# Kernel tuning notes

Hardware: AMD Instinct MI355X
Metric: run time of the kernel (lower is better)

Reference implementation:

```python
import jax, jax.numpy as jnp
import numpy as np

H, W, WS = 48, 48, 8          # spatial grid and window radius
D, NUM_HEADS = 256, 8          # embed dim, heads
N = H * W
K = (2 * WS + 1) ** 2          # max neighbors = 289
EPS = 1e-5


def _precompute_neighbors(h, w, ws):
    """Faithful port of SCAM._precompute_neighbors (pads ragged rows with n[0])."""
    neighbors_list = []
    for idx in range(h * w):
        row, col = idx // w, idx % w
        nb = []
        for i in range(-ws, ws + 1):
            for j in range(-ws, ws + 1):
                r, c = row + i, col + j
                if 0 <= r < h and 0 <= c < w:
                    nb.append(r * w + c)
        neighbors_list.append(nb)
    max_n = max(len(n) for n in neighbors_list)
    padded = np.array([n + [n[0]] * (max_n - len(n)) for n in neighbors_list], dtype=np.int32)
    return padded


def setup_inputs() -> dict:
    key = jax.random.key(0)
    k1, k2, k3, k4 = jax.random.split(key, 4)
    B = 1
    scale = 0.02
    return {
        "x1": jax.random.normal(k1, (B, N, D), dtype=jnp.float32),
        "x2": jax.random.normal(k2, (B, N, D), dtype=jnp.float32),
        "ln_gamma": jnp.ones((D,), jnp.float32),
        "ln_beta": jnp.zeros((D,), jnp.float32),
        "in_proj_w": jax.random.normal(k3, (3 * D, D), dtype=jnp.float32) * scale,
        "in_proj_b": jnp.zeros((3 * D,), jnp.float32),
        "out_w": jax.random.normal(k4, (D, D), dtype=jnp.float32) * scale,
        "out_b": jnp.zeros((D,), jnp.float32),
        "neighbors_idx": jnp.asarray(_precompute_neighbors(H, W, WS)),  # [N, K] int32
    }


def _layernorm(x, gamma, beta):
    mu = jnp.mean(x, axis=-1, keepdims=True)
    var = jnp.var(x, axis=-1, keepdims=True)
    return (x - mu) * jax.lax.rsqrt(var + EPS) * gamma + beta


def reference(x1, x2, ln_gamma, ln_beta, in_proj_w, in_proj_b, out_w, out_b, neighbors_idx):
    B, n, d = x1.shape
    hd = d // NUM_HEADS

    # --- neighborhood gather-attention on x2 ---
    neighbor_feats = x2[:, neighbors_idx, :]                         # [B, N, K, D]
    scores = jnp.einsum('bnd,bnkd->bnk', x2, neighbor_feats) / (d ** 0.5)
    attn_w = jax.nn.softmax(scores, axis=-1)                          # softmax over neighbors
    x2_fused = jnp.einsum('bnk,bnkd->bnd', attn_w, neighbor_feats)    # [B, N, D]
    x2_fused = _layernorm(x2_fused, ln_gamma, ln_beta)

    # --- standard MHA: query=x2_fused, key=value=x1 ---
    wq, wk, wv = in_proj_w[:d], in_proj_w[d:2 * d], in_proj_w[2 * d:]
    bq, bk, bv = in_proj_b[:d], in_proj_b[d:2 * d], in_proj_b[2 * d:]
    q = (x2_fused @ wq.T + bq).reshape(B, n, NUM_HEADS, hd).transpose(0, 2, 1, 3)
    k = (x1 @ wk.T + bk).reshape(B, n, NUM_HEADS, hd).transpose(0, 2, 1, 3)
    v = (x1 @ wv.T + bv).reshape(B, n, NUM_HEADS, hd).transpose(0, 2, 1, 3)
    logits = jnp.einsum('bhqd,bhkd->bhqk', q, k) / (hd ** 0.5)        # [B, H, N, N]
    p = jax.nn.softmax(logits, axis=-1)
    o = jnp.einsum('bhqk,bhkd->bhqd', p, v)                           # [B, H, N, hd]
    o = o.transpose(0, 2, 1, 3).reshape(B, n, d)
    return o @ out_w.T + out_b
```

## Files before the change

### kernel.cpp

```cpp
#include <hip/hip_runtime.h>
#include <math.h>

#define N 2304
#define D 256
#define K_NB 289
#define NH 8
#define HD 32
#define KS 8
#define SEG (N / KS)
#define NGR 2320

typedef __attribute__((ext_vector_type(8))) short short8;
typedef __attribute__((ext_vector_type(4))) short bf16x4;
typedef __attribute__((ext_vector_type(4))) float floatx4;

static __device__ __forceinline__ unsigned short f2bf(float x) {
  union { float f; unsigned u; } v; v.f = x;
  unsigned r = (v.u + 0x7fffu + ((v.u >> 16) & 1u)) >> 16;
  return (unsigned short)r;
}
static __device__ __forceinline__ unsigned pack2bf(float lo, float hi) {
  return (unsigned)f2bf(lo) | ((unsigned)f2bf(hi) << 16);
}

__global__ __launch_bounds__(256) void prep_kernel(
    const float* __restrict__ x2, unsigned short* __restrict__ x2b_full,
    unsigned short* __restrict__ x2t_full)
{
  __shared__ unsigned short T[16][17];
  const int tx = threadIdx.x & 15;
  const int ty = threadIdx.x >> 4;
  const int k0 = blockIdx.x * 16;
  const int f0 = blockIdx.y * 16;
  const int key = k0 + ty - 8;
  unsigned short v = 0;
  if (key >= 0 && key < N) v = f2bf(x2[(size_t)key * D + f0 + tx]);
  x2b_full[(size_t)(k0 + ty) * D + f0 + tx] = v;
  T[ty][tx] = v;
  __syncthreads();
  x2t_full[(size_t)(f0 + ty) * NGR + k0 + tx] = T[tx][ty];
}

__global__ __launch_bounds__(256) void stage1_mfma_kernel(
    const unsigned short* __restrict__ x2b,
    const unsigned short* __restrict__ x2t,
    const float* __restrict__ gamma, const float* __restrict__ beta,
    float* __restrict__ x2f)
{
  __shared__ float S[16][548];
  __shared__ __align__(16) unsigned short Pb[16][552];
  __shared__ float dinv[16];
  __shared__ float lr1[4][16], lr2[4][16];

  const int t    = threadIdx.x;
  const int w    = t >> 6;
  const int lane = t & 63;
  const int g    = lane >> 4;
  const int cL   = lane & 15;
  const int b  = blockIdx.x;
  const int r  = b / 3;
  const int c0 = (b % 3) * 16;
  const int qbase = r * 48 + c0;
  const int row_lo = max(0, 8 - r);
  const int row_hi = min(16, 55 - r);

  short8 qf[8];
  {
    const unsigned short* qptr = x2b + (size_t)(qbase + cL) * D + g * 8;
    #pragma unroll
    for (int s = 0; s < 8; ++s) qf[s] = *(const short8*)(qptr + s * 32);
  }

  for (int wr = row_lo + w; wr <= row_hi; wr += 4) {
    const int kr = r - 8 + wr;
    const int keybase = kr * 48 + c0 - 8;
    #pragma unroll
    for (int ch = 0; ch < 2; ++ch) {
      const unsigned short* kptr = x2b + (size_t)(keybase + ch * 16 + cL) * D + g * 8;
      floatx4 sa = {0.f, 0.f, 0.f, 0.f};
      #pragma unroll
      for (int s = 0; s < 8; ++s) {
        const short8 kf = *(const short8*)(kptr + s * 32);
        sa = __builtin_amdgcn_mfma_f32_16x16x32_bf16(qf[s], kf, sa, 0, 0, 0);
      }
      #pragma unroll
      for (int reg = 0; reg < 4; ++reg)
        S[g * 4 + reg][wr * 32 + ch * 16 + cL] = sa[reg] * 0.0625f;
    }
  }
  __syncthreads();

  if (t < 16) {
    const int c = c0 + t;
    const int nrows = min(r + 8, 47) - max(r - 8, 0) + 1;
    const int ncols = min(c + 8, 47) - max(c - 8, 0) + 1;
    const int mult  = K_NB - nrows * ncols + 1;
    if (mult > 1) {
      const int wr0 = max(0, 8 - r);
      const int wc0 = (c >= 8) ? t : (8 - c0);
      S[t][wr0 * 32 + wc0] += __logf((float)mult);
    }
  }
  __syncthreads();

  {
    const int qi = t >> 4, ti = t & 15;
    float ssum = 0.f;
    for (int wk = ti; wk < 544; wk += 16) {
      const int wr = wk >> 5, wc = wk & 31;
      const int kr = r - 8 + wr;
      const int kc = c0 - 8 + wc;
      const bool valid = (kr >= 0) & (kr < 48) & (kc >= 0) & (kc < 48) &
                         (wc >= qi) & (wc <= qi + 16);
      const float p = valid ? __expf(S[qi][wk]) : 0.f;
      ssum += p;
      Pb[qi][wk] = valid ? f2bf(p) : (unsigned short)0;
    }
    #pragma unroll
    for (int off = 1; off <= 8; off <<= 1) ssum += __shfl_xor(ssum, off);
    if (ti == 0) dinv[qi] = 1.f / ssum;
  }
  __syncthreads();

  floatx4 acc[4];
  #pragma unroll
  for (int ng = 0; ng < 4; ++ng) acc[ng] = (floatx4){0.f, 0.f, 0.f, 0.f};
  const int fb = w * 64;
  for (int wr = row_lo; wr <= row_hi; ++wr) {
    const int keybase = (r - 8 + wr) * 48 + c0 - 8;
    const short8 pA = *(const short8*)&Pb[cL][wr * 32 + g * 8];
    #pragma unroll
    for (int ng = 0; ng < 4; ++ng) {
      const short8 vf = *(const short8*)(x2t + (size_t)(fb + ng * 16 + cL) * NGR + keybase + g * 8);
      acc[ng] = __builtin_amdgcn_mfma_f32_16x16x32_bf16(pA, vf, acc[ng], 0, 0, 0);
    }
  }

  float vout[4][4], ps1[4] = {0,0,0,0}, ps2[4] = {0,0,0,0};
  #pragma unroll
  for (int reg = 0; reg < 4; ++reg) {
    const float di = dinv[g * 4 + reg];
    #pragma unroll
    for (int ng = 0; ng < 4; ++ng) {
      const float v = acc[ng][reg] * di;
      vout[ng][reg] = v;
      ps1[reg] += v;
      ps2[reg] += v * v;
    }
  }
  #pragma unroll
  for (int off = 1; off <= 8; off <<= 1) {
    #pragma unroll
    for (int reg = 0; reg < 4; ++reg) {
      ps1[reg] += __shfl_xor(ps1[reg], off);
      ps2[reg] += __shfl_xor(ps2[reg], off);
    }
  }
  if (cL == 0) {
    #pragma unroll
    for (int reg = 0; reg < 4; ++reg) {
      lr1[w][g * 4 + reg] = ps1[reg];
      lr2[w][g * 4 + reg] = ps2[reg];
    }
  }
  __syncthreads();
  #pragma unroll
  for (int reg = 0; reg < 4; ++reg) {
    const int m = g * 4 + reg;
    const float s1 = lr1[0][m] + lr1[1][m] + lr1[2][m] + lr1[3][m];
    const float s2 = lr2[0][m] + lr2[1][m] + lr2[2][m] + lr2[3][m];
    const float mu  = s1 * (1.f / 256.f);
    const float var = s2 * (1.f / 256.f) - mu * mu;
    const float rs  = rsqrtf(var + 1e-5f);
    #pragma unroll
    for (int ng = 0; ng < 4; ++ng) {
      const int f = fb + ng * 16 + cL;
      x2f[(size_t)(qbase + m) * D + f] = (vout[ng][reg] - mu) * rs * gamma[f] + beta[f];
    }
  }
}

__global__ __launch_bounds__(256) void gemm_qkv_kernel(
    const float* __restrict__ A0, const float* __restrict__ A1,
    const float* __restrict__ W, const float* __restrict__ bias,
    unsigned short* __restrict__ Qb, unsigned short* __restrict__ Kb,
    unsigned short* __restrict__ Vtb)
{
  __shared__ float As[64][68];
  __shared__ float Ws[64][68];
  const int t  = threadIdx.x;
  const int tx = t & 15;
  const int ty = t >> 4;
  const int j0 = blockIdx.x * 64;
  const int m0 = blockIdx.y * 64;
  const float* __restrict__ Asrc = (j0 < 256) ? A0 : A1;

  float acc[4][4];
  #pragma unroll
  for (int r = 0; r < 4; ++r)
    #pragma unroll
    for (int c = 0; c < 4; ++c) acc[r][c] = 0.f;

  for (int kc = 0; kc < D; kc += 64) {
    const int col = tx * 4;
    #pragma unroll
    for (int i = 0; i < 4; ++i) {
      const int r = ty + 16 * i;
      *(float4*)&As[r][col] = *(const float4*)(Asrc + (size_t)(m0 + r) * D + kc + col);
      *(float4*)&Ws[r][col] = *(const float4*)(W    + (size_t)(j0 + r) * D + kc + col);
    }
    __syncthreads();
    #pragma unroll 4
    for (int kk = 0; kk < 64; kk += 4) {
      float4 a4[4], b4[4];
      #pragma unroll
      for (int r = 0; r < 4; ++r) a4[r] = *(const float4*)&As[ty * 4 + r][kk];
      #pragma unroll
      for (int c = 0; c < 4; ++c) b4[c] = *(const float4*)&Ws[tx + 16 * c][kk];
      #pragma unroll
      for (int r = 0; r < 4; ++r)
        #pragma unroll
        for (int c = 0; c < 4; ++c) {
          acc[r][c] += a4[r].x * b4[c].x;
          acc[r][c] += a4[r].y * b4[c].y;
          acc[r][c] += a4[r].z * b4[c].z;
          acc[r][c] += a4[r].w * b4[c].w;
        }
    }
    __syncthreads();
  }
  const float qscale = 0.17677669529663687f;
  #pragma unroll
  for (int r = 0; r < 4; ++r) {
    const int m = m0 + ty * 4 + r;
    #pragma unroll
    for (int c = 0; c < 4; ++c) {
      const int j = j0 + tx + 16 * c;
      const float v = acc[r][c] + bias[j];
      if (j0 < 256)       Qb[(size_t)m * D + j] = f2bf(v * qscale);
      else if (j0 < 512)  Kb[(size_t)m * D + (j - 256)] = f2bf(v);
      else                Vtb[(size_t)(j - 512) * N + m] = f2bf(v);
    }
  }
}

__global__ __launch_bounds__(128) void attn_mfma_kernel(
    const unsigned short* __restrict__ Qb, const unsigned short* __restrict__ Kb,
    const unsigned short* __restrict__ Vtb,
    float* __restrict__ pacc, float* __restrict__ psum)
{
  __shared__ __align__(16) unsigned short Ksh[2][32 * 40];
  __shared__ __align__(16) unsigned short Vsh[2][32 * 40];

  const int t    = threadIdx.x;
  const int wv   = t >> 6;
  const int lane = t & 63;
  const int g    = lane >> 4;
  const int c    = lane & 15;
  const int seg  = blockIdx.x;
  const int qb   = blockIdx.y;
  const int head = blockIdx.z;
  const int q0w  = qb * 128 + wv * 64;
  const int key0 = seg * SEG;

  short8 qf[4];
  #pragma unroll
  for (int qt = 0; qt < 4; ++qt)
    qf[qt] = *(const short8*)(Qb + (size_t)(q0w + qt * 16 + c) * D + head * HD + g * 8);

  const unsigned short* ksrc = Kb  + (size_t)(key0 + t / 4) * D + head * HD + (t % 4) * 8;
  const unsigned short* vsrc = Vtb + (size_t)(head * HD + t / 4) * N + key0 + (t % 4) * 8;
  const int sdst = (t / 4) * 40 + (t % 4) * 8;

  {
    const float4 gk = *(const float4*)ksrc;
    const float4 gv = *(const float4*)vsrc;
    *(float4*)&Ksh[0][sdst] = gk;
    *(float4*)&Vsh[0][sdst] = gv;
  }
  __syncthreads();

  floatx4 accL[4], accH[4];
  float ssum[4];
  #pragma unroll
  for (int qt = 0; qt < 4; ++qt) {
    accL[qt] = (floatx4){0.f, 0.f, 0.f, 0.f};
    accH[qt] = (floatx4){0.f, 0.f, 0.f, 0.f};
    ssum[qt] = 0.f;
  }

  const int NCH = SEG / 32;
  for (int ch = 0; ch < NCH; ++ch) {
    float4 gk, gv;
    const bool more = (ch + 1 < NCH);
    if (more) {
      gk = *(const float4*)(ksrc + (size_t)(ch + 1) * 32 * D);
      gv = *(const float4*)(vsrc + (ch + 1) * 32);
    }
    const unsigned short* kb = Ksh[ch & 1];
    const unsigned short* vb = Vsh[ch & 1];

    #pragma unroll
    for (int kk = 0; kk < 2; ++kk) {
      const short8 kf  = *(const short8*)&kb[(kk * 16 + c) * 40 + g * 8];
      const bf16x4 vf0 = *(const bf16x4*)&vb[c * 40 + kk * 16 + g * 4];
      const bf16x4 vf1 = *(const bf16x4*)&vb[(16 + c) * 40 + kk * 16 + g * 4];
      #pragma unroll
      for (int qt = 0; qt < 4; ++qt) {
        const floatx4 z = {0.f, 0.f, 0.f, 0.f};
        floatx4 sA = __builtin_amdgcn_mfma_f32_16x16x32_bf16(kf, qf[qt], z, 0, 0, 0);
        const float p0 = __expf(sA[0]);
        const float p1 = __expf(sA[1]);
        const float p2 = __expf(sA[2]);
        const float p3 = __expf(sA[3]);
        ssum[qt] += (p0 + p1) + (p2 + p3);
        union { unsigned u[2]; bf16x4 s; } pB;
        pB.u[0] = pack2bf(p0, p1);
        pB.u[1] = pack2bf(p2, p3);
        accL[qt] = __builtin_amdgcn_mfma_f32_16x16x16bf16_1k(vf0, pB.s, accL[qt], 0, 0, 0);
        accH[qt] = __builtin_amdgcn_mfma_f32_16x16x16bf16_1k(vf1, pB.s, accH[qt], 0, 0, 0);
      }
    }
    if (more) {
      *(float4*)&Ksh[(ch + 1) & 1][sdst] = gk;
      *(float4*)&Vsh[(ch + 1) & 1][sdst] = gv;
    }
    __syncthreads();
  }

  #pragma unroll
  for (int qt = 0; qt < 4; ++qt) {
    float s = ssum[qt];
    s += __shfl_xor(s, 16);
    s += __shfl_xor(s, 32);
    const size_t row = (size_t)(seg * NH + head) * N + q0w + qt * 16 + c;
    *(float4*)(pacc + row * HD + g * 4) =
        make_float4(accL[qt][0], accL[qt][1], accL[qt][2], accL[qt][3]);
    *(float4*)(pacc + row * HD + 16 + g * 4) =
        make_float4(accH[qt][0], accH[qt][1], accH[qt][2], accH[qt][3]);
    if (g == 0) psum[row] = s;
  }
}

__global__ __launch_bounds__(256) void combine_kernel(
    const float* __restrict__ pacc, const float* __restrict__ psum,
    float* __restrict__ o)
{
  const int n = blockIdx.x;
  const int t = threadIdx.x;
  const int h = t >> 5;
  const int d = t & 31;
  float num = 0.f, den = 0.f;
  #pragma unroll
  for (int sgi = 0; sgi < KS; ++sgi) {
    const size_t b = (size_t)(sgi * NH + h) * N + n;
    num += pacc[b * HD + d];
    den += psum[b];
  }
  o[(size_t)n * D + t] = num / den;
}

__global__ __launch_bounds__(256) void gemm_kernel(
    const float* __restrict__ A, const float* __restrict__ W,
    const float* __restrict__ bias, float* __restrict__ C)
{
  __shared__ float As[64][68];
  __shared__ float Ws[64][68];
  const int t  = threadIdx.x;
  const int tx = t & 15;
  const int ty = t >> 4;
  const int j0 = blockIdx.x * 64;
  const int m0 = blockIdx.y * 64;

  float acc[4][4];
  #pragma unroll
  for (int r = 0; r < 4; ++r)
    #pragma unroll
    for (int c = 0; c < 4; ++c) acc[r][c] = 0.f;

  for (int kc = 0; kc < D; kc += 64) {
    const int col = tx * 4;
    #pragma unroll
    for (int i = 0; i < 4; ++i) {
      const int r = ty + 16 * i;
      *(float4*)&As[r][col] = *(const float4*)(A + (size_t)(m0 + r) * D + kc + col);
      *(float4*)&Ws[r][col] = *(const float4*)(W + (size_t)(j0 + r) * D + kc + col);
    }
    __syncthreads();
    #pragma unroll 4
    for (int kk = 0; kk < 64; kk += 4) {
      float4 a4[4], b4[4];
      #pragma unroll
      for (int r = 0; r < 4; ++r) a4[r] = *(const float4*)&As[ty * 4 + r][kk];
      #pragma unroll
      for (int c = 0; c < 4; ++c) b4[c] = *(const float4*)&Ws[tx + 16 * c][kk];
      #pragma unroll
      for (int r = 0; r < 4; ++r)
        #pragma unroll
        for (int c = 0; c < 4; ++c) {
          acc[r][c] += a4[r].x * b4[c].x;
          acc[r][c] += a4[r].y * b4[c].y;
          acc[r][c] += a4[r].z * b4[c].z;
          acc[r][c] += a4[r].w * b4[c].w;
        }
    }
    __syncthreads();
  }
  #pragma unroll
  for (int r = 0; r < 4; ++r) {
    const int m = m0 + ty * 4 + r;
    #pragma unroll
    for (int c = 0; c < 4; ++c) {
      const int j = j0 + tx + 16 * c;
      C[(size_t)m * D + j] = acc[r][c] + bias[j];
    }
  }
}

extern "C" void kernel_launch(void* const* d_in, const int* in_sizes, int n_in,
                              void* d_out, int out_size, void* d_ws, size_t ws_size,
                              hipStream_t stream)
{
  (void)in_sizes; (void)n_in; (void)out_size; (void)ws_size;
  const float* x1  = (const float*)d_in[0];
  const float* x2  = (const float*)d_in[1];
  const float* lng = (const float*)d_in[2];
  const float* lnb = (const float*)d_in[3];
  const float* ipw = (const float*)d_in[4];
  const float* ipb = (const float*)d_in[5];
  const float* ow  = (const float*)d_in[6];
  const float* ob  = (const float*)d_in[7];
  float* out = (float*)d_out;

  char* p = (char*)d_ws;
  float* x2f  = (float*)p; p += (size_t)N * D * 4;
  float* o    = (float*)p; p += (size_t)N * D * 4;
  float* pacc = (float*)p; p += (size_t)KS * NH * N * HD * 4;
  float* psum = (float*)p; p += (size_t)KS * NH * N * 4;
  unsigned short* Qb  = (unsigned short*)p; p += (size_t)N * D * 2;
  unsigned short* Kb  = (unsigned short*)p; p += (size_t)N * D * 2;
  unsigned short* Vtb = (unsigned short*)p; p += (size_t)D * N * 2;
  unsigned short* x2b_full = (unsigned short*)p; p += (size_t)NGR * D * 2;
  unsigned short* x2t_full = (unsigned short*)p; p += (size_t)D * NGR * 2;
  const unsigned short* x2b = x2b_full + (size_t)8 * D;
  const unsigned short* x2t = x2t_full + 8;

  prep_kernel<<<dim3(NGR / 16, 16), 256, 0, stream>>>(x2, x2b_full, x2t_full);
  stage1_mfma_kernel<<<144, 256, 0, stream>>>(x2b, x2t, lng, lnb, x2f);
  gemm_qkv_kernel<<<dim3(12, 36), 256, 0, stream>>>(x2f, x1, ipw, ipb, Qb, Kb, Vtb);
  attn_mfma_kernel<<<dim3(KS, N / 128, NH), 128, 0, stream>>>(Qb, Kb, Vtb, pacc, psum);
  combine_kernel<<<N, 256, 0, stream>>>(pacc, psum, o);
  gemm_kernel<<<dim3(4, 36), 256, 0, stream>>>(o, ow, ob, out);
}
```

Measured before the change: 165.6 us.

## Replace FP32 SIMT GEMMs with split-bf16 three-pass MFMA GEMMs; widen stage1 to 512 threads

The QKV and output projections move from scalar FP32 shared-memory GEMMs to bf16 MFMA GEMMs. Each operand is split into high and low bf16 parts, and three passes (hh, lh, hl) recover near-FP32 accuracy. A new conversion kernel splits x1 and both weight matrices every call. Stage1 and combine now write hi/lo bf16 outputs directly. Stage1 also doubles to 512 threads, giving each wave a 32-feature slice, which adds an extra launch and more memory traffic in exchange for matrix-core throughput.

```diff
diff --git a/kernel.cpp b/kernel.cpp
--- a/kernel.cpp
+++ b/kernel.cpp
@@ -19,8 +19,33 @@
   unsigned r = (v.u + 0x7fffu + ((v.u >> 16) & 1u)) >> 16;
   return (unsigned short)r;
 }
+static __device__ __forceinline__ float bf2f(unsigned short h) {
+  union { unsigned u; float f; } v; v.u = (unsigned)h << 16;
+  return v.f;
+}
 static __device__ __forceinline__ unsigned pack2bf(float lo, float hi) {
   return (unsigned)f2bf(lo) | ((unsigned)f2bf(hi) << 16);
+}
+
+#define CV_X1 (N * D)
+#define CV_W  (768 * 256)
+#define CV_OW (256 * 256)
+__global__ __launch_bounds__(256) void conv_hilo_kernel(
+    const float* __restrict__ x1, const float* __restrict__ ipw,
+    const float* __restrict__ ow,
+    unsigned short* __restrict__ x1h, unsigned short* __restrict__ x1l,
+    unsigned short* __restrict__ wh,  unsigned short* __restrict__ wl,
+    unsigned short* __restrict__ owh, unsigned short* __restrict__ owl)
+{
+  int i = blockIdx.x * 256 + threadIdx.x;
+  const float* src; unsigned short *dh, *dl; int off;
+  if (i < CV_X1)            { src = x1;  dh = x1h; dl = x1l; off = i; }
+  else if (i < CV_X1 + CV_W){ src = ipw; dh = wh;  dl = wl;  off = i - CV_X1; }
+  else                      { src = ow;  dh = owh; dl = owl; off = i - CV_X1 - CV_W; }
+  const float v = src[off];
+  const unsigned short h = f2bf(v);
+  dh[off] = h;
+  dl[off] = f2bf(v - bf2f(h));
 }
 
 __global__ __launch_bounds__(256) void prep_kernel(
@@ -41,16 +66,16 @@
   x2t_full[(size_t)(f0 + ty) * NGR + k0 + tx] = T[tx][ty];
 }
 
-__global__ __launch_bounds__(256) void stage1_mfma_kernel(
+__global__ __launch_bounds__(512) void stage1_mfma_kernel(
     const unsigned short* __restrict__ x2b,
     const unsigned short* __restrict__ x2t,
     const float* __restrict__ gamma, const float* __restrict__ beta,
-    float* __restrict__ x2f)
+    unsigned short* __restrict__ x2fh, unsigned short* __restrict__ x2fl)
 {
   __shared__ float S[16][548];
   __shared__ __align__(16) unsigned short Pb[16][552];
   __shared__ float dinv[16];
-  __shared__ float lr1[4][16], lr2[4][16];
+  __shared__ float lr1[8][16], lr2[8][16];
 
   const int t    = threadIdx.x;
   const int w    = t >> 6;
@@ -71,7 +96,7 @@
     for (int s = 0; s < 8; ++s) qf[s] = *(const short8*)(qptr + s * 32);
   }
 
-  for (int wr = row_lo + w; wr <= row_hi; wr += 4) {
+  for (int wr = row_lo + w; wr <= row_hi; wr += 8) {
     const int kr = r - 8 + wr;
     const int keybase = kr * 48 + c0 - 8;
     #pragma unroll
@@ -104,9 +129,9 @@
   __syncthreads();
 
   {
-    const int qi = t >> 4, ti = t & 15;
+    const int qi = t >> 5, ti = t & 31;
     float ssum = 0.f;
-    for (int wk = ti; wk < 544; wk += 16) {
+    for (int wk = ti; wk < 544; wk += 32) {
       const int wr = wk >> 5, wc = wk & 31;
       const int kr = r - 8 + wr;
       const int kc = c0 - 8 + wc;
@@ -117,31 +142,31 @@
       Pb[qi][wk] = valid ? f2bf(p) : (unsigned short)0;
     }
     #pragma unroll
-    for (int off = 1; off <= 8; off <<= 1) ssum += __shfl_xor(ssum, off);
+    for (int off = 1; off <= 16; off <<= 1) ssum += __shfl_xor(ssum, off);
     if (ti == 0) dinv[qi] = 1.f / ssum;
   }
   __syncthreads();
 
-  floatx4 acc[4];
-  #pragma unroll
-  for (int ng = 0; ng < 4; ++ng) acc[ng] = (floatx4){0.f, 0.f, 0.f, 0.f};
-  const int fb = w * 64;
+  floatx4 acc[2];
+  acc[0] = (floatx4){0.f, 0.f, 0.f, 0.f};
+  acc[1] = (floatx4){0.f, 0.f, 0.f, 0.f};
+  const int fb = w * 32;
   for (int wr = row_lo; wr <= row_hi; ++wr) {
     const int keybase = (r - 8 + wr) * 48 + c0 - 8;
     const short8 pA = *(const short8*)&Pb[cL][wr * 32 + g * 8];
     #pragma unroll
-    for (int ng = 0; ng < 4; ++ng) {
+    for (int ng = 0; ng < 2; ++ng) {
       const short8 vf = *(const short8*)(x2t + (size_t)(fb + ng * 16 + cL) * NGR + keybase + g * 8);
       acc[ng] = __builtin_amdgcn_mfma_f32_16x16x32_bf16(pA, vf, acc[ng], 0, 0, 0);
     }
   }
 
-  float vout[4][4], ps1[4] = {0,0,0,0}, ps2[4] = {0,0,0,0};
+  float vout[2][4], ps1[4] = {0,0,0,0}, ps2[4] = {0,0,0,0};
   #pragma unroll
   for (int reg = 0; reg < 4; ++reg) {
     const float di = dinv[g * 4 + reg];
     #pragma unroll
-    for (int ng = 0; ng < 4; ++ng) {
+    for (int ng = 0; ng < 2; ++ng) {
       const float v = acc[ng][reg] * di;
       vout[ng][reg] = v;
       ps1[reg] += v;
@@ -167,79 +192,81 @@
   #pragma unroll
   for (int reg = 0; reg < 4; ++reg) {
     const int m = g * 4 + reg;
-    const float s1 = lr1[0][m] + lr1[1][m] + lr1[2][m] + lr1[3][m];
-    const float s2 = lr2[0][m] + lr2[1][m] + lr2[2][m] + lr2[3][m];
+    float s1 = 0.f, s2 = 0.f;
+    #pragma unroll
+    for (int ww = 0; ww < 8; ++ww) { s1 += lr1[ww][m]; s2 += lr2[ww][m]; }
     const float mu  = s1 * (1.f / 256.f);
     const float var = s2 * (1.f / 256.f) - mu * mu;
     const float rs  = rsqrtf(var + 1e-5f);
     #pragma unroll
-    for (int ng = 0; ng < 4; ++ng) {
+    for (int ng = 0; ng < 2; ++ng) {
       const int f = fb + ng * 16 + cL;
-      x2f[(size_t)(qbase + m) * D + f] = (vout[ng][reg] - mu) * rs * gamma[f] + beta[f];
-    }
-  }
-}
-
-__global__ __launch_bounds__(256) void gemm_qkv_kernel(
-    const float* __restrict__ A0, const float* __restrict__ A1,
-    const float* __restrict__ W, const float* __restrict__ bias,
+      const float val = (vout[ng][reg] - mu) * rs * gamma[f] + beta[f];
+      const unsigned short h = f2bf(val);
+      const size_t idx = (size_t)(qbase + m) * D + f;
+      x2fh[idx] = h;
+      x2fl[idx] = f2bf(val - bf2f(h));
+    }
+  }
+}
+
+__global__ __launch_bounds__(256) void gemm_qkv_mfma(
+    const unsigned short* __restrict__ x2fh, const unsigned short* __restrict__ x2fl,
+    const unsigned short* __restrict__ x1h,  const unsigned short* __restrict__ x1l,
+    const unsigned short* __restrict__ Wh,   const unsigned short* __restrict__ Wl,
+    const float* __restrict__ bias,
     unsigned short* __restrict__ Qb, unsigned short* __restrict__ Kb,
     unsigned short* __restrict__ Vtb)
 {
-  __shared__ float As[64][68];
-  __shared__ float Ws[64][68];
-  const int t  = threadIdx.x;
-  const int tx = t & 15;
-  const int ty = t >> 4;
-  const int j0 = blockIdx.x * 64;
+  const int t = threadIdx.x;
+  const int wv = t >> 6, lane = t & 63, g = lane >> 4, c = lane & 15;
+  const int n0 = blockIdx.x * 128;
   const int m0 = blockIdx.y * 64;
-  const float* __restrict__ Asrc = (j0 < 256) ? A0 : A1;
-
-  float acc[4][4];
-  #pragma unroll
-  for (int r = 0; r < 4; ++r)
-    #pragma unroll
-    for (int c = 0; c < 4; ++c) acc[r][c] = 0.f;
-
-  for (int kc = 0; kc < D; kc += 64) {
-    const int col = tx * 4;
-    #pragma unroll
-    for (int i = 0; i < 4; ++i) {
-      const int r = ty + 16 * i;
-      *(float4*)&As[r][col] = *(const float4*)(Asrc + (size_t)(m0 + r) * D + kc + col);
-      *(float4*)&Ws[r][col] = *(const float4*)(W    + (size_t)(j0 + r) * D + kc + col);
-    }
-    __syncthreads();
-    #pragma unroll 4
-    for (int kk = 0; kk < 64; kk += 4) {
-      float4 a4[4], b4[4];
-      #pragma unroll
-      for (int r = 0; r < 4; ++r) a4[r] = *(const float4*)&As[ty * 4 + r][kk];
-      #pragma unroll
-      for (int c = 0; c < 4; ++c) b4[c] = *(const float4*)&Ws[tx + 16 * c][kk];
-      #pragma unroll
-      for (int r = 0; r < 4; ++r)
+  const int nw = n0 + wv * 32;
+  const unsigned short* Ah = (n0 < 256) ? x2fh : x1h;
+  const unsigned short* Al = (n0 < 256) ? x2fl : x1l;
+
+  floatx4 acc[4][2];
+  #pragma unroll
+  for (int mt = 0; mt < 4; ++mt)
+    #pragma unroll
+    for (int nt = 0; nt < 2; ++nt) acc[mt][nt] = (floatx4){0.f, 0.f, 0.f, 0.f};
+
+  #pragma unroll
+  for (int pass = 0; pass < 3; ++pass) {
+    const unsigned short* Ap = (pass == 1) ? Al : Ah;
+    const unsigned short* Wp = (pass == 2) ? Wl : Wh;
+    for (int kc = 0; kc < 256; kc += 32) {
+      short8 af[4], bf[2];
+      #pragma unroll
+      for (int mt = 0; mt < 4; ++mt)
+        af[mt] = *(const short8*)(Ap + (size_t)(m0 + mt * 16 + c) * 256 + kc + g * 8);
+      #pragma unroll
+      for (int nt = 0; nt < 2; ++nt)
+        bf[nt] = *(const short8*)(Wp + (size_t)(nw + nt * 16 + c) * 256 + kc + g * 8);
+      #pragma unroll
+      for (int mt = 0; mt < 4; ++mt)
         #pragma unroll
-        for (int c = 0; c < 4; ++c) {
-          acc[r][c] += a4[r].x * b4[c].x;
-          acc[r][c] += a4[r].y * b4[c].y;
-          acc[r][c] += a4[r].z * b4[c].z;
-          acc[r][c] += a4[r].w * b4[c].w;
-        }
-    }
-    __syncthreads();
-  }
+        for (int nt = 0; nt < 2; ++nt)
+          acc[mt][nt] = __builtin_amdgcn_mfma_f32_16x16x32_bf16(af[mt], bf[nt], acc[mt][nt], 0, 0, 0);
+    }
+  }
+
   const float qscale = 0.17677669529663687f;
   #pragma unroll
-  for (int r = 0; r < 4; ++r) {
-    const int m = m0 + ty * 4 + r;
-    #pragma unroll
-    for (int c = 0; c < 4; ++c) {
-      const int j = j0 + tx + 16 * c;
-      const float v = acc[r][c] + bias[j];
-      if (j0 < 256)       Qb[(size_t)m * D + j] = f2bf(v * qscale);
-      else if (j0 < 512)  Kb[(size_t)m * D + (j - 256)] = f2bf(v);
-      else                Vtb[(size_t)(j - 512) * N + m] = f2bf(v);
+  for (int mt = 0; mt < 4; ++mt) {
+    #pragma unroll
+    for (int nt = 0; nt < 2; ++nt) {
+      const int j = nw + nt * 16 + c;
+      const float bj = bias[j];
+      #pragma unroll
+      for (int r = 0; r < 4; ++r) {
+        const int m = m0 + mt * 16 + 4 * g + r;
+        const float v = acc[mt][nt][r] + bj;
+        if (j < 256)       Qb[(size_t)m * 256 + j] = f2bf(v * qscale);
+        else if (j < 512)  Kb[(size_t)m * 256 + (j - 256)] = f2bf(v);
+        else               Vtb[(size_t)(j - 512) * N + m] = f2bf(v);
+      }
     }
   }
 }
@@ -344,7 +371,7 @@
 
 __global__ __launch_bounds__(256) void combine_kernel(
     const float* __restrict__ pacc, const float* __restrict__ psum,
-    float* __restrict__ o)
+    unsigned short* __restrict__ oh, unsigned short* __restrict__ ol)
 {
   const int n = blockIdx.x;
   const int t = threadIdx.x;
@@ -357,62 +384,61 @@
     num += pacc[b * HD + d];
     den += psum[b];
   }
-  o[(size_t)n * D + t] = num / den;
-}
-
-__global__ __launch_bounds__(256) void gemm_kernel(
-    const float* __restrict__ A, const float* __restrict__ W,
-    const float* __restrict__ bias, float* __restrict__ C)
-{
-  __shared__ float As[64][68];
-  __shared__ float Ws[64][68];
-  const int t  = threadIdx.x;
-  const int tx = t & 15;
-  const int ty = t >> 4;
-  const int j0 = blockIdx.x * 64;
+  const float v = num / den;
+  const unsigned short hh = f2bf(v);
+  const size_t idx = (size_t)n * D + t;
+  oh[idx] = hh;
+  ol[idx] = f2bf(v - bf2f(hh));
+}
+
+__global__ __launch_bounds__(256) void gemm_out_mfma(
+    const unsigned short* __restrict__ oh, const unsigned short* __restrict__ ol,
+    const unsigned short* __restrict__ Wh, const unsigned short* __restrict__ Wl,
+    const float* __restrict__ bias, float* __restrict__ out)
+{
+  const int t = threadIdx.x;
+  const int wv = t >> 6, lane = t & 63, g = lane >> 4, c = lane & 15;
+  const int n0 = blockIdx.x * 128;
   const int m0 = blockIdx.y * 64;
-
-  float acc[4][4];
-  #pragma unroll
-  for (int r = 0; r < 4; ++r)
-    #pragma unroll
-    for (int c = 0; c < 4; ++c) acc[r][c] = 0.f;
-
-  for (int kc = 0; kc < D; kc += 64) {
-    const int col = tx * 4;
-    #pragma unroll
-    for (int i = 0; i < 4; ++i) {
-      const int r = ty + 16 * i;
-      *(float4*)&As[r][col] = *(const float4*)(A + (size_t)(m0 + r) * D + kc + col);
-      *(float4*)&Ws[r][col] = *(const float4*)(W + (size_t)(j0 + r) * D + kc + col);
-    }
-    __syncthreads();
-    #pragma unroll 4
-    for (int kk = 0; kk < 64; kk += 4) {
-      float4 a4[4], b4[4];
-      #pragma unroll
-      for (int r = 0; r < 4; ++r) a4[r] = *(const float4*)&As[ty * 4 + r][kk];
-      #pragma unroll
-      for (int c = 0; c < 4; ++c) b4[c] = *(const float4*)&Ws[tx + 16 * c][kk];
-      #pragma unroll
-      for (int r = 0; r < 4; ++r)
+  const int nw = n0 + wv * 32;
+
+  floatx4 acc[4][2];
+  #pragma unroll
+  for (int mt = 0; mt < 4; ++mt)
+    #pragma unroll
+    for (int nt = 0; nt < 2; ++nt) acc[mt][nt] = (floatx4){0.f, 0.f, 0.f, 0.f};
+
+  #pragma unroll
+  for (int pass = 0; pass < 3; ++pass) {
+    const unsigned short* Ap = (pass == 1) ? ol : oh;
+    const unsigned short* Wp = (pass == 2) ? Wl : Wh;
+    for (int kc = 0; kc < 256; kc += 32) {
+      short8 af[4], bf[2];
+      #pragma unroll
+      for (int mt = 0; mt < 4; ++mt)
+        af[mt] = *(const short8*)(Ap + (size_t)(m0 + mt * 16 + c) * 256 + kc + g * 8);
+      #pragma unroll
+      for (int nt = 0; nt < 2; ++nt)
+        bf[nt] = *(const short8*)(Wp + (size_t)(nw + nt * 16 + c) * 256 + kc + g * 8);
+      #pragma unroll
+      for (int mt = 0; mt < 4; ++mt)
         #pragma unroll
-        for (int c = 0; c < 4; ++c) {
-          acc[r][c] += a4[r].x * b4[c].x;
-          acc[r][c] += a4[r].y * b4[c].y;
-          acc[r][c] += a4[r].z * b4[c].z;
-          acc[r][c] += a4[r].w * b4[c].w;
-        }
-    }
-    __syncthreads();
-  }
-  #pragma unroll
-  for (int r = 0; r < 4; ++r) {
-    const int m = m0 + ty * 4 + r;
-    #pragma unroll
-    for (int c = 0; c < 4; ++c) {
-      const int j = j0 + tx + 16 * c;
-      C[(size_t)m * D + j] = acc[r][c] + bias[j];
+        for (int nt = 0; nt < 2; ++nt)
+          acc[mt][nt] = __builtin_amdgcn_mfma_f32_16x16x32_bf16(af[mt], bf[nt], acc[mt][nt], 0, 0, 0);
+    }
+  }
+
+  #pragma unroll
+  for (int mt = 0; mt < 4; ++mt) {
+    #pragma unroll
+    for (int nt = 0; nt < 2; ++nt) {
+      const int j = nw + nt * 16 + c;
+      const float bj = bias[j];
+      #pragma unroll
+      for (int r = 0; r < 4; ++r) {
+        const int m = m0 + mt * 16 + 4 * g + r;
+        out[(size_t)m * 256 + j] = acc[mt][nt][r] + bj;
+      }
     }
   }
 }
@@ -433,22 +459,33 @@
   float* out = (float*)d_out;
 
   char* p = (char*)d_ws;
-  float* x2f  = (float*)p; p += (size_t)N * D * 4;
-  float* o    = (float*)p; p += (size_t)N * D * 4;
   float* pacc = (float*)p; p += (size_t)KS * NH * N * HD * 4;
   float* psum = (float*)p; p += (size_t)KS * NH * N * 4;
-  unsigned short* Qb  = (unsigned short*)p; p += (size_t)N * D * 2;
-  unsigned short* Kb  = (unsigned short*)p; p += (size_t)N * D * 2;
-  unsigned short* Vtb = (unsigned short*)p; p += (size_t)D * N * 2;
+  unsigned short* Qb   = (unsigned short*)p; p += (size_t)N * D * 2;
+  unsigned short* Kb   = (unsigned short*)p; p += (size_t)N * D * 2;
+  unsigned short* Vtb  = (unsigned short*)p; p += (size_t)D * N * 2;
   unsigned short* x2b_full = (unsigned short*)p; p += (size_t)NGR * D * 2;
   unsigned short* x2t_full = (unsigned short*)p; p += (size_t)D * NGR * 2;
+  unsigned short* x1h  = (unsigned short*)p; p += (size_t)N * D * 2;
+  unsigned short* x1l  = (unsigned short*)p; p += (size_t)N * D * 2;
+  unsigned short* wh   = (unsigned short*)p; p += (size_t)768 * 256 * 2;
+  unsigned short* wl   = (unsigned short*)p; p += (size_t)768 * 256 * 2;
+  unsigned short* owh  = (unsigned short*)p; p += (size_t)256 * 256 * 2;
+  unsigned short* owl  = (unsigned short*)p; p += (size_t)256 * 256 * 2;
+  unsigned short* x2fh = (unsigned short*)p; p += (size_t)N * D * 2;
+  unsigned short* x2fl = (unsigned short*)p; p += (size_t)N * D * 2;
+  unsigned short* oh   = (unsigned short*)p; p += (size_t)N * D * 2;
+  unsigned short* ol   = (unsigned short*)p; p += (size_t)N * D * 2;
   const unsigned short* x2b = x2b_full + (size_t)8 * D;
   const unsigned short* x2t = x2t_full + 8;
 
+  conv_hilo_kernel<<<(CV_X1 + CV_W + CV_OW) / 256, 256, 0, stream>>>(
+      x1, ipw, ow, x1h, x1l, wh, wl, owh, owl);
   prep_kernel<<<dim3(NGR / 16, 16), 256, 0, stream>>>(x2, x2b_full, x2t_full);
-  stage1_mfma_kernel<<<144, 256, 0, stream>>>(x2b, x2t, lng, lnb, x2f);
-  gemm_qkv_kernel<<<dim3(12, 36), 256, 0, stream>>>(x2f, x1, ipw, ipb, Qb, Kb, Vtb);
+  stage1_mfma_kernel<<<144, 512, 0, stream>>>(x2b, x2t, lng, lnb, x2fh, x2fl);
+  gemm_qkv_mfma<<<dim3(6, 36), 256, 0, stream>>>(
+      x2fh, x2fl, x1h, x1l, wh, wl, ipb, Qb, Kb, Vtb);
   attn_mfma_kernel<<<dim3(KS, N / 128, NH), 128, 0, stream>>>(Qb, Kb, Vtb, pacc, psum);
-  combine_kernel<<<N, 256, 0, stream>>>(pacc, psum, o);
-  gemm_kernel<<<dim3(4, 36), 256, 0, stream>>>(o, ow, ob, out);
-}
+  combine_kernel<<<N, 256, 0, stream>>>(pacc, psum, oh, ol);
+  gemm_out_mfma<<<dim3(2, 36), 256, 0, stream>>>(oh, ol, owh, owl, ob, out);
+}
```

Result: faster. 161.1 us (-2.7%).
